# Kernel tuning notes

Hardware: AMD Instinct MI355X
Metric: run time of the kernel (lower is better)

## Reference

```python
import jax, jax.numpy as jnp
import numpy as np
import math

V, B, C, H, W, D, G, N = 4, 2, 32, 128, 128, 32, 8, 4
ATTN_TEMP = 2.0


def _bilinear_sample(img, gx, gy):
    """img: (C,Hs,Ws); gx,gy: (P,) normalized coords in [-1,1].
    PyTorch grid_sample(mode=bilinear, padding=zeros, align_corners=True)."""
    Cc, Hs, Ws = img.shape
    x = (gx + 1.0) * 0.5 * (Ws - 1)
    y = (gy + 1.0) * 0.5 * (Hs - 1)
    x0 = jnp.floor(x)
    y0 = jnp.floor(y)
    wx = x - x0
    wy = y - y0
    x0i = x0.astype(jnp.int32)
    y0i = y0.astype(jnp.int32)

    def gather(xi, yi):
        valid = ((xi >= 0) & (xi < Ws) & (yi >= 0) & (yi < Hs)).astype(img.dtype)
        v = img[:, jnp.clip(yi, 0, Hs - 1), jnp.clip(xi, 0, Ws - 1)]
        return v * valid

    v00 = gather(x0i, y0i)
    v01 = gather(x0i + 1, y0i)
    v10 = gather(x0i, y0i + 1)
    v11 = gather(x0i + 1, y0i + 1)
    return (v00 * (1 - wx) + v01 * wx) * (1 - wy) + (v10 * (1 - wx) + v11 * wx) * wy


_bilinear_batched = jax.vmap(_bilinear_sample)  # over batch


def _homo_warp(src_fea, src_proj, ref_proj, depth):
    """src_fea (B,C,Hs,Ws), projs (B,4,4), depth (B,D,H,W) -> (B,C,D,H,W)."""
    Bb, Cc, Hs, Ws = src_fea.shape
    Dd, Hr, Wr = depth.shape[1], depth.shape[2], depth.shape[3]
    proj = src_proj @ jnp.linalg.inv(ref_proj)
    rot = proj[:, :3, :3]
    trans = proj[:, :3, 3]  # (B,3)
    yy, xx = jnp.meshgrid(jnp.arange(Hr, dtype=jnp.float32),
                          jnp.arange(Wr, dtype=jnp.float32), indexing='ij')
    xyz = jnp.stack([xx.ravel(), yy.ravel(), jnp.ones(Hr * Wr, jnp.float32)], 0)  # (3,P)
    rot_xyz = jnp.einsum('bij,jp->bip', rot, xyz)  # (B,3,P)
    pts = rot_xyz[:, :, None, :] * depth.reshape(Bb, 1, Dd, Hr * Wr) \
          + trans[:, :, None, None]  # (B,3,D,P)
    z = pts[:, 2]
    z = jnp.where(z == 0.0, 1e-9, z)
    gx = pts[:, 0] / z / ((Ws - 1) / 2.0) - 1.0  # (B,D,P)
    gy = pts[:, 1] / z / ((Hs - 1) / 2.0) - 1.0
    # grid built under torch.no_grad in the original
    gx = jax.lax.stop_gradient(gx).reshape(Bb, Dd * Hr * Wr)
    gy = jax.lax.stop_gradient(gy).reshape(Bb, Dd * Hr * Wr)
    warped = _bilinear_batched(src_fea, gx, gy)  # (B,C,D*P)
    return warped.reshape(Bb, Cc, Dd, Hr, Wr)


def setup_inputs() -> dict:
    key = jax.random.key(0)
    ks = jax.random.split(key, 6)
    ref_features = jax.random.normal(ks[0], (V, B, C, H, W), jnp.float32)
    src_features = jax.random.normal(ks[1], (V, B, C, H, W), jnp.float32)
    # structured camera matrices: [.,.,0]=extrinsic, [.,.,1]=intrinsic
    f = 100.0
    K = np.eye(4, dtype=np.float32)
    K[0, 0] = f; K[1, 1] = f; K[0, 2] = W / 2.0; K[1, 2] = H / 2.0
    projs = np.zeros((B, V + 1, 2, 4, 4), np.float32)
    for v in range(V + 1):
        ang = 0.0 if v == 0 else 0.02 * v
        ca, sa = math.cos(ang), math.sin(ang)
        E = np.eye(4, dtype=np.float32)
        E[:3, :3] = np.array([[ca, 0, sa], [0, 1, 0], [-sa, 0, ca]], np.float32)
        E[0, 3] = 0.0 if v == 0 else 5.0 * v
        projs[:, v, 0] = E
        projs[:, v, 1] = K
    proj_matrices = jnp.asarray(projs)
    dvals = jnp.linspace(425.0, 935.0, D, dtype=jnp.float32)
    depth_hypo = dvals[None, :, None, None] * jnp.ones((B, D, H, W), jnp.float32)
    sample_grids = 2.0 * jax.random.uniform(ks[2], (V, B, N, H, W, 2), jnp.float32) - 1.0
    w_reg = jax.random.normal(ks[3], (G,), jnp.float32) * 0.1
    w_enh = jax.random.normal(ks[4], (G, G * N), jnp.float32) * 0.05
    return {
        'ref_features': ref_features,
        'src_features': src_features,
        'proj_matrices': proj_matrices,
        'depth_hypo': depth_hypo,
        'sample_grids': sample_grids,
        'w_reg': w_reg,
        'w_enh': w_enh,
        'group_cor_dim': G,
        'stage_idx': 3,
    }


def reference(ref_features, src_features, proj_matrices, depth_hypo,
              sample_grids, w_reg, w_enh, group_cor_dim, stage_idx):
    Bb, Dd, Hh, Ww = depth_hypo.shape
    Cc = ref_features.shape[2]
    Gg = group_cor_dim
    ref_proj = proj_matrices[:, 0]
    ref_proj_new = ref_proj[:, 0].at[:, :3, :4].set(
        jnp.einsum('bij,bjk->bik', ref_proj[:, 1, :3, :3], ref_proj[:, 0, :3, :4]))
    cor_weight_sum = 1e-8
    cor_feats = 0.0
    cor_weights = []
    for src_idx in range(V):
        src_proj = proj_matrices[:, src_idx + 1]
        src_proj_new = src_proj[:, 0].at[:, :3, :4].set(
            jnp.einsum('bij,bjk->bik', src_proj[:, 1, :3, :3], src_proj[:, 0, :3, :4]))
        warped_src = _homo_warp(src_features[src_idx], src_proj_new, ref_proj_new,
                                depth_hypo)  # (B,C,D,H,W)
        ref_vol = ref_features[src_idx][:, :, None].reshape(Bb, Gg, Cc // Gg, 1, Hh, Ww)
        wsrc = warped_src.reshape(Bb, Gg, Cc // Gg, Dd, Hh, Ww)
        cor_feat = (wsrc * ref_vol).mean(2)  # (B,G,D,H,W) group correlation
        # --- regcorr: second grid_sample along epipolar-line samples ---
        cf = cor_feat.reshape(Bb, Gg * Dd, Hh, Ww)
        grids = sample_grids[src_idx].reshape(Bb, N * Hh * Ww, 2)
        cf_s = _bilinear_batched(cf, grids[..., 0], grids[..., 1])  # (B,G*D,N*H*W)
        cf_s = cf_s.reshape(Bb, Gg, Dd, N, Hh, Ww)
        cf_s = jnp.transpose(cf_s, (0, 1, 3, 2, 4, 5)).reshape(Bb, Gg * N, Dd, Hh, Ww)
        # line_cross_enhanced_net stand-in: learned mix of line samples, residual add
        cor_feat = cor_feat + jnp.einsum('gk,bkdhw->bgdhw', w_enh, cf_s)
        # --- attn_fuse_d softmax fusion across depth ---
        cor_weight = jax.nn.softmax(cor_feat.sum(1) / ATTN_TEMP, axis=1) / math.sqrt(Cc)
        cor_weight_sum = cor_weight_sum + cor_weight
        cor_weights.append(cor_weight.max(1))
        cor_feats = cor_feats + cor_weight[:, None] * cor_feat
    cor_feats = cor_feats / cor_weight_sum[:, None]
    # regnet stand-in: linear reduction over group dim
    attn_logits = jnp.einsum('g,bgdhw->bdhw', w_reg, cor_feats)
    attn_weight = jax.nn.softmax(attn_logits, axis=1)
    idx = jnp.argmax(attn_weight, axis=1)  # (B,H,W)
    depth = jnp.take_along_axis(depth_hypo, idx[:, None], axis=1)[:, 0]
    # stage_idx=3 -> interpolate scale_factor=1 (identity)
    photometric_confidence = attn_weight.max(1)
    return depth, photometric_confidence, attn_weight, jnp.stack(cor_weights)
```

## Files before the change

kernel.cpp:

```cpp
#include <hip/hip_runtime.h>

#define Vv 4
#define Bn 2
#define Cn 32
#define Hn 128
#define Wn 128
#define Dn 32
#define Gn 8
#define Nn 4
#define HW (Hn*Wn)
#define BHW (Bn*Hn*Wn)
#define DHW (Dn*Hn*Wn)
#define BDHW (Bn*Dn*Hn*Wn)
#define NBLK (DHW/256)
#define RBLK (Gn*HW/256)

__global__ void setup_proj(const float* __restrict__ pm,
                           const float* __restrict__ wenh,
                           const float* __restrict__ wreg,
                           double* __restrict__ projws,
                           double* __restrict__ wtab) {
    int t = threadIdx.x;
    if (t < Gn) wtab[t] = (double)wreg[t];
    if (t < Gn * Nn) {
        double a = 0.0, c = 0.0;
        for (int g = 0; g < Gn; g++) {
            double wv = (double)wenh[g * (Gn * Nn) + t];
            a += wv;
            c += (double)wreg[g] * wv;
        }
        wtab[8 + t] = a; wtab[40 + t] = c;
    }
    if (t >= Vv * Bn) return;
    int v = t / Bn, b = t % Bn;
    const float* Eref = pm + (((size_t)b * (Vv + 1) + 0) * 2 + 0) * 16;
    const float* Kref = pm + (((size_t)b * (Vv + 1) + 0) * 2 + 1) * 16;
    const float* Esrc = pm + (((size_t)b * (Vv + 1) + (v + 1)) * 2 + 0) * 16;
    const float* Ksrc = pm + (((size_t)b * (Vv + 1) + (v + 1)) * 2 + 1) * 16;
    double R[16], S[16];
    for (int r = 0; r < 3; r++)
        for (int c = 0; c < 4; c++) {
            R[r*4+c] = (double)Kref[r*4+0]*Eref[0*4+c] + (double)Kref[r*4+1]*Eref[1*4+c] + (double)Kref[r*4+2]*Eref[2*4+c];
            S[r*4+c] = (double)Ksrc[r*4+0]*Esrc[0*4+c] + (double)Ksrc[r*4+1]*Esrc[1*4+c] + (double)Ksrc[r*4+2]*Esrc[2*4+c];
        }
    for (int c = 0; c < 4; c++) { R[12+c] = Eref[12+c]; S[12+c] = Esrc[12+c]; }
    double M[4][8];
    for (int r = 0; r < 4; r++)
        for (int c = 0; c < 4; c++) { M[r][c] = R[r*4+c]; M[r][4+c] = (r == c) ? 1.0 : 0.0; }
    for (int col = 0; col < 4; col++) {
        int piv = col; double best = fabs(M[col][col]);
        for (int r = col+1; r < 4; r++) { double a = fabs(M[r][col]); if (a > best) { best = a; piv = r; } }
        if (piv != col)
            for (int c = 0; c < 8; c++) { double tmp = M[col][c]; M[col][c] = M[piv][c]; M[piv][c] = tmp; }
        double inv = 1.0 / M[col][col];
        for (int c = 0; c < 8; c++) M[col][c] *= inv;
        for (int r = 0; r < 4; r++) if (r != col) {
            double f = M[r][col];
            for (int c = 0; c < 8; c++) M[r][c] -= f * M[col][c];
        }
    }
    double P[16];
    for (int r = 0; r < 4; r++)
        for (int c = 0; c < 4; c++) {
            double acc = 0.0;
            for (int k = 0; k < 4; k++) acc += S[r*4+k] * M[k][4+c];
            P[r*4+c] = acc;
        }
    double* o = projws + t * 12;
    o[0]=P[0];  o[1]=P[1];  o[2]=P[2];
    o[3]=P[4];  o[4]=P[5];  o[5]=P[6];
    o[6]=P[8];  o[7]=P[9];  o[8]=P[10];
    o[9]=P[3];  o[10]=P[7]; o[11]=P[11];
}

__device__ __forceinline__ void repack_body(
    int tid, const float* __restrict__ srcf, const float* __restrict__ reff,
    float4* __restrict__ qsrc, float4* __restrict__ qref, int v, int b)
{
    int p = tid & (HW - 1);
    int g = tid >> 14;
    const float* sb = srcf + ((size_t)(v*Bn + b)) * Cn * HW + (size_t)(g*4) * HW + p;
    const float* rb = reff + ((size_t)(v*Bn + b)) * Cn * HW + (size_t)(g*4) * HW + p;
    float4 s4; s4.x = sb[0]; s4.y = sb[HW]; s4.z = sb[2*HW]; s4.w = sb[3*HW];
    float4 r4; r4.x = rb[0]; r4.y = rb[HW]; r4.z = rb[2*HW]; r4.w = rb[3*HW];
    qsrc[(size_t)g * HW + p] = s4;
    qref[(size_t)g * HW + p] = r4;
}

__device__ __forceinline__ void warp_body_q(
    int tid, const float4* __restrict__ qsrc, const float4* __restrict__ qref,
    const float* __restrict__ dh, const double* __restrict__ projws,
    const float* sU1, const float* sU2, const float* sR,
    float2* __restrict__ ownbuf, float2* __restrict__ tapbuf, int v, int b)
{
    int d = tid & 31, p = tid >> 5;
    int w = p & 127, h = p >> 7;
    const double* pr = projws + (v * Bn + b) * 12;
    double depth = (double)dh[(size_t)(b * Dn + d) * HW + p];
    double xf = (double)w, yf = (double)h;
    double px = (pr[0]*xf + pr[1]*yf + pr[2]) * depth + pr[9];
    double py = (pr[3]*xf + pr[4]*yf + pr[5]) * depth + pr[10];
    double pz = (pr[6]*xf + pr[7]*yf + pr[8]) * depth + pr[11];
    if (pz == 0.0) pz = 1e-9;
    double invz = 1.0 / pz;
    double xs = px * invz;
    double ys = py * invz;
    double x0f = floor(xs), y0f = floor(ys);
    double wx = xs - x0f, wy = ys - y0f;
    int ix = (int)x0f, iy = (int)y0f;
    bool vx0 = (ix >= 0) && (ix < Wn), vx1 = (ix + 1 >= 0) && (ix + 1 < Wn);
    bool vy0 = (iy >= 0) && (iy < Hn), vy1 = (iy + 1 >= 0) && (iy + 1 < Hn);
    int cx0 = min(max(ix, 0), Wn-1), cx1 = min(max(ix+1, 0), Wn-1);
    int cy0 = min(max(iy, 0), Hn-1), cy1 = min(max(iy+1, 0), Hn-1);
    float a00 = (vx0 && vy0) ? (float)((1.0-wx)*(1.0-wy)) : 0.f;
    float a01 = (vx1 && vy0) ? (float)(wx*(1.0-wy))       : 0.f;
    float a10 = (vx0 && vy1) ? (float)((1.0-wx)*wy)       : 0.f;
    float a11 = (vx1 && vy1) ? (float)(wx*wy)             : 0.f;
    int o00 = cy0*Wn + cx0, o01 = cy0*Wn + cx1, o10 = cy1*Wn + cx0, o11 = cy1*Wn + cx1;
    float cor[Gn];
    #pragma unroll
    for (int j = 0; j < Gn; j++) {
        const float4* qs = qsrc + (size_t)j * HW;
        float4 t00 = qs[o00], t01 = qs[o01], t10 = qs[o10], t11 = qs[o11];
        float4 rr = qref[(size_t)j * HW + p];
        float vx = a00*t00.x + a01*t01.x + a10*t10.x + a11*t11.x;
        float vy = a00*t00.y + a01*t01.y + a10*t10.y + a11*t11.y;
        float vz = a00*t00.z + a01*t01.z + a10*t10.z + a11*t11.z;
        float vw = a00*t00.w + a01*t01.w + a10*t10.w + a11*t11.w;
        cor[j] = ((vx*rr.x + vy*rr.y) + vz*rr.z) + vw*rr.w;
    }
    float s_own = 0.f, r_own = 0.f;
    #pragma unroll
    for (int g = 0; g < Gn; g++) { s_own += cor[g]; r_own += sR[g] * cor[g]; }
    float2 o2; o2.x = 0.25f * s_own; o2.y = 0.25f * r_own;
    ownbuf[tid] = o2;
    #pragma unroll
    for (int n = 0; n < Nn; n++) {
        float t1 = 0.f, t2 = 0.f;
        #pragma unroll
        for (int g = 0; g < Gn; g++) {
            t1 += sU1[g*Nn + n] * cor[g];
            t2 += sU2[g*Nn + n] * cor[g];
        }
        float2 t; t.x = 0.25f * t1; t.y = 0.25f * t2;
        tapbuf[((size_t)p * Nn + n) * Dn + d] = t;
    }
}

__device__ __forceinline__ void warp_body(
    int tid, const float* __restrict__ srcf, const float* __restrict__ reff,
    const float* __restrict__ dh, const double* __restrict__ projws,
    const float* sU1, const float* sU2, const float* sR,
    float2* __restrict__ ownbuf, float2* __restrict__ tapbuf, int v, int b)
{
    int d = tid & 31, p = tid >> 5;
    int w = p & 127, h = p >> 7;
    const double* pr = projws + (v * Bn + b) * 12;
    double depth = (double)dh[(size_t)(b * Dn + d) * HW + p];
    double xf = (double)w, yf = (double)h;
    double px = (pr[0]*xf + pr[1]*yf + pr[2]) * depth + pr[9];
    double py = (pr[3]*xf + pr[4]*yf + pr[5]) * depth + pr[10];
    double pz = (pr[6]*xf + pr[7]*yf + pr[8]) * depth + pr[11];
    if (pz == 0.0) pz = 1e-9;
    double invz = 1.0 / pz;
    double xs = px * invz;
    double ys = py * invz;
    double x0f = floor(xs), y0f = floor(ys);
    double wx = xs - x0f, wy = ys - y0f;
    int ix = (int)x0f, iy = (int)y0f;
    bool vx0 = (ix >= 0) && (ix < Wn), vx1 = (ix + 1 >= 0) && (ix + 1 < Wn);
    bool vy0 = (iy >= 0) && (iy < Hn), vy1 = (iy + 1 >= 0) && (iy + 1 < Hn);
    int cx0 = min(max(ix, 0), Wn-1), cx1 = min(max(ix+1, 0), Wn-1);
    int cy0 = min(max(iy, 0), Hn-1), cy1 = min(max(iy+1, 0), Hn-1);
    float a00 = (vx0 && vy0) ? (float)((1.0-wx)*(1.0-wy)) : 0.f;
    float a01 = (vx1 && vy0) ? (float)(wx*(1.0-wy))       : 0.f;
    float a10 = (vx0 && vy1) ? (float)((1.0-wx)*wy)       : 0.f;
    float a11 = (vx1 && vy1) ? (float)(wx*wy)             : 0.f;
    int o00 = cy0*Wn + cx0, o01 = cy0*Wn + cx1, o10 = cy1*Wn + cx0, o11 = cy1*Wn + cx1;
    const float* sb = srcf + ((size_t)(v*Bn + b)) * Cn * HW;
    const float* rb = reff + ((size_t)(v*Bn + b)) * Cn * HW + p;
    float cor[Gn];
    #pragma unroll
    for (int g = 0; g < Gn; g++) cor[g] = 0.f;
    #pragma unroll
    for (int c = 0; c < Cn; c++) {
        const float* sc = sb + c * HW;
        float val = a00*sc[o00] + a01*sc[o01] + a10*sc[o10] + a11*sc[o11];
        cor[c >> 2] += val * rb[c * HW];
    }
    float s_own = 0.f, r_own = 0.f;
    #pragma unroll
    for (int g = 0; g < Gn; g++) { s_own += cor[g]; r_own += sR[g] * cor[g]; }
    float2 o2; o2.x = 0.25f * s_own; o2.y = 0.25f * r_own;
    ownbuf[tid] = o2;
    #pragma unroll
    for (int n = 0; n < Nn; n++) {
        float t1 = 0.f, t2 = 0.f;
        #pragma unroll
        for (int g = 0; g < Gn; g++) {
            t1 += sU1[g*Nn + n] * cor[g];
            t2 += sU2[g*Nn + n] * cor[g];
        }
        float2 t; t.x = 0.25f * t1; t.y = 0.25f * t2;
        tapbuf[((size_t)p * Nn + n) * Dn + d] = t;
    }
}

template <int MODE>
__device__ __forceinline__ void sample_body(
    int tid, const float2* __restrict__ ownbuf, const float2* __restrict__ tapbuf,
    const float* __restrict__ grids, float2* __restrict__ accf,
    float* __restrict__ out_corw, const float* __restrict__ depth_hypo,
    float* __restrict__ out, int v, int b)
{
    int d = tid & 31;
    int p = tid >> 5;
    int w = p & 127, h = p >> 7;

    float2 ow = ownbuf[tid];
    double s = (double)ow.x, r = (double)ow.y;

    const float2* gb2 = (const float2*)(grids + ((size_t)(v*Bn + b)) * Nn * HW * 2);
    #pragma unroll
    for (int n = 0; n < Nn; n++) {
        float2 g2 = gb2[((size_t)n * Hn + h) * Wn + w];
        double gx = (double)g2.x, gy = (double)g2.y;
        double xs = (gx + 1.0) * 63.5;
        double ys = (gy + 1.0) * 63.5;
        double x0f = floor(xs), y0f = floor(ys);
        double wx = xs - x0f, wy = ys - y0f;
        int ix = (int)x0f, iy = (int)y0f;
        bool vx0 = (ix >= 0) && (ix < Wn), vx1 = (ix + 1 >= 0) && (ix + 1 < Wn);
        bool vy0 = (iy >= 0) && (iy < Hn), vy1 = (iy + 1 >= 0) && (iy + 1 < Hn);
        int cx0 = min(max(ix, 0), Wn-1), cx1 = min(max(ix+1, 0), Wn-1);
        int cy0 = min(max(iy, 0), Hn-1), cy1 = min(max(iy+1, 0), Hn-1);
        double a00 = (vx0 && vy0) ? (1.0-wx)*(1.0-wy) : 0.0;
        double a01 = (vx1 && vy0) ? wx*(1.0-wy)       : 0.0;
        double a10 = (vx0 && vy1) ? (1.0-wx)*wy       : 0.0;
        double a11 = (vx1 && vy1) ? wx*wy             : 0.0;
        float2 q00 = tapbuf[((size_t)(cy0*Wn + cx0) * Nn + n) * Dn + d];
        float2 q01 = tapbuf[((size_t)(cy0*Wn + cx1) * Nn + n) * Dn + d];
        float2 q10 = tapbuf[((size_t)(cy1*Wn + cx0) * Nn + n) * Dn + d];
        float2 q11 = tapbuf[((size_t)(cy1*Wn + cx1) * Nn + n) * Dn + d];
        s += a00*(double)q00.x + a01*(double)q01.x + a10*(double)q10.x + a11*(double)q11.x;
        r += a00*(double)q00.y + a01*(double)q01.y + a10*(double)q10.y + a11*(double)q11.y;
    }
    double logit = s * 0.5;
    double m = logit;
    #pragma unroll
    for (int mask = 16; mask >= 1; mask >>= 1) m = fmax(m, __shfl_xor(m, mask));
    double e = exp(logit - m);
    double ssum = e;
    #pragma unroll
    for (int mask = 16; mask >= 1; mask >>= 1) ssum += __shfl_xor(ssum, mask);
    const double SQRTC = 5.656854249492381;
    double cw = e / ssum / SQRTC;
    if (d == 0) out_corw[(size_t)v * BHW + (size_t)b * HW + p] = (float)(1.0 / ssum / SQRTC);

    if (MODE == 0) {
        float2 a; a.x = (float)(1e-8 + cw); a.y = (float)(cw * r);
        accf[tid] = a;
    } else if (MODE == 1) {
        float2 a = accf[tid];
        a.x = (float)((double)a.x + cw);
        a.y = (float)((double)a.y + cw * r);
        accf[tid] = a;
    } else {
        float2 a = accf[tid];
        double cs = (double)a.x + cw;
        double wr = (double)a.y + cw * r;
        double lg = wr / cs;
        double fm = lg;
        #pragma unroll
        for (int mask = 16; mask >= 1; mask >>= 1) fm = fmax(fm, __shfl_xor(fm, mask));
        double fe = exp(lg - fm);
        double fsum = fe;
        #pragma unroll
        for (int mask = 16; mask >= 1; mask >>= 1) fsum += __shfl_xor(fsum, mask);
        out[2*BHW + (size_t)b * DHW + (size_t)d * HW + p] = (float)(fe / fsum);
        double bv = lg; int bi = d;
        #pragma unroll
        for (int mask = 16; mask >= 1; mask >>= 1) {
            double ov = __shfl_xor(bv, mask);
            int oi = __shfl_xor(bi, mask);
            if (ov > bv || (ov == bv && oi < bi)) { bv = ov; bi = oi; }
        }
        double rv = (d == bi) ? -1e300 : lg; int ri = d;
        #pragma unroll
        for (int mask = 16; mask >= 1; mask >>= 1) {
            double ov = __shfl_xor(rv, mask);
            int oi = __shfl_xor(ri, mask);
            if (ov > rv || (ov == rv && oi < ri)) { rv = ov; ri = oi; }
        }
        if (d == 0) {
            const float* dhb = depth_hypo + (size_t)b * DHW + p;
            double eps = 5e-3 * (1.0 + fabs(bv));
            bool adj = (ri == bi + 1) || (ri == bi - 1);
            float dep;
            if (adj && (bv - rv) <= eps)
                dep = 0.5f * (dhb[(size_t)bi * HW] + dhb[(size_t)ri * HW]);
            else
                dep = dhb[(size_t)bi * HW];
            out[(size_t)b * HW + p] = dep;
            out[BHW + (size_t)b * HW + p] = (float)(1.0 / fsum);
        }
    }
}

__global__ __launch_bounds__(256) void repack_k(
    const float* __restrict__ srcf, const float* __restrict__ reff,
    float4* __restrict__ qsrc, float4* __restrict__ qref, int v, int b)
{
    repack_body(blockIdx.x * 256 + threadIdx.x, srcf, reff, qsrc, qref, v, b);
}

__global__ __launch_bounds__(256) void warp0_q(
    const float* __restrict__ srcf, const float* __restrict__ reff,
    const float4* __restrict__ qsrcR, const float4* __restrict__ qrefR,
    float4* __restrict__ qsrcW, float4* __restrict__ qrefW,
    const float* __restrict__ dh, const double* __restrict__ projws,
    const double* __restrict__ wtab,
    float2* __restrict__ ownbuf, float2* __restrict__ tapbuf)
{
    int lt = threadIdx.x;
    if (blockIdx.x < NBLK) {
        __shared__ float sU1[Gn * Nn], sU2[Gn * Nn], sR[Gn];
        if (lt < Gn * Nn) { sU1[lt] = (float)wtab[8 + lt]; sU2[lt] = (float)wtab[40 + lt]; }
        if (lt < Gn) sR[lt] = (float)wtab[lt];
        __syncthreads();
        warp_body_q(blockIdx.x * 256 + lt, qsrcR, qrefR, dh, projws,
                    sU1, sU2, sR, ownbuf, tapbuf, 0, 0);
    } else {
        repack_body((blockIdx.x - NBLK) * 256 + lt, srcf, reff, qsrcW, qrefW, 1, 0);
    }
}

__global__ __launch_bounds__(256) void warp_corr(
    const float* __restrict__ srcf, const float* __restrict__ reff,
    const float* __restrict__ dh, const double* __restrict__ projws,
    const double* __restrict__ wtab,
    float2* __restrict__ ownbuf, float2* __restrict__ tapbuf, int v, int b)
{
    __shared__ float sU1[Gn * Nn], sU2[Gn * Nn], sR[Gn];
    int lt = threadIdx.x;
    if (lt < Gn * Nn) { sU1[lt] = (float)wtab[8 + lt]; sU2[lt] = (float)wtab[40 + lt]; }
    if (lt < Gn) sR[lt] = (float)wtab[lt];
    __syncthreads();
    warp_body(blockIdx.x * 256 + lt, srcf, reff, dh, projws, sU1, sU2, sR,
              ownbuf, tapbuf, v, b);
}

template <int MODE>
__global__ __launch_bounds__(256) void sample_enh(
    const float2* __restrict__ ownbuf, const float2* __restrict__ tapbuf,
    const float* __restrict__ grids, float2* __restrict__ accf,
    float* __restrict__ out_corw, const float* __restrict__ depth_hypo,
    float* __restrict__ out, int v, int b)
{
    sample_body<MODE>(blockIdx.x * 256 + threadIdx.x, ownbuf, tapbuf, grids,
                      accf, out_corw, depth_hypo, out, v, b);
}

template <int MODE>
__global__ __launch_bounds__(256) void fused_swq(
    const float* __restrict__ srcf, const float* __restrict__ reff,
    const float4* __restrict__ qsrcR, const float4* __restrict__ qrefR,
    float4* __restrict__ qsrcW, float4* __restrict__ qrefW,
    const float* __restrict__ dh, const double* __restrict__ projws,
    const double* __restrict__ wtab, const float* __restrict__ grids,
    const float2* __restrict__ ownR, const float2* __restrict__ tapR,
    float2* __restrict__ ownW, float2* __restrict__ tapW,
    float2* __restrict__ accf, float* __restrict__ out_corw,
    float* __restrict__ out, int vs, int bs, int vw, int bw, int vr, int br)
{
    int lt = threadIdx.x;
    if (blockIdx.x >= 2*NBLK) {
        repack_body((blockIdx.x - 2*NBLK) * 256 + lt, srcf, reff, qsrcW, qrefW, vr, br);
        return;
    }
    int role = blockIdx.x & 1;
    int vb   = blockIdx.x >> 1;
    if (role == 0) {
        sample_body<MODE>(vb * 256 + lt, ownR, tapR, grids,
                          accf, out_corw, dh, out, vs, bs);
    } else {
        __shared__ float sU1[Gn * Nn], sU2[Gn * Nn], sR[Gn];
        if (lt < Gn * Nn) { sU1[lt] = (float)wtab[8 + lt]; sU2[lt] = (float)wtab[40 + lt]; }
        if (lt < Gn) sR[lt] = (float)wtab[lt];
        __syncthreads();
        warp_body_q(vb * 256 + lt, qsrcR, qrefR, dh, projws,
                    sU1, sU2, sR, ownW, tapW, vw, bw);
    }
}

template <int MODE>
__global__ __launch_bounds__(256) void fused_sw(
    const float* __restrict__ srcf, const float* __restrict__ reff,
    const float* __restrict__ dh, const double* __restrict__ projws,
    const double* __restrict__ wtab, const float* __restrict__ grids,
    const float2* __restrict__ ownR, const float2* __restrict__ tapR,
    float2* __restrict__ ownW, float2* __restrict__ tapW,
    float2* __restrict__ accf, float* __restrict__ out_corw,
    float* __restrict__ out, int vs, int bs, int vw, int bw)
{
    int lt = threadIdx.x;
    int role = blockIdx.x & 1;
    int vb   = blockIdx.x >> 1;
    if (role == 0) {
        sample_body<MODE>(vb * 256 + lt, ownR, tapR, grids,
                          accf, out_corw, dh, out, vs, bs);
    } else {
        __shared__ float sU1[Gn * Nn], sU2[Gn * Nn], sR[Gn];
        if (lt < Gn * Nn) { sU1[lt] = (float)wtab[8 + lt]; sU2[lt] = (float)wtab[40 + lt]; }
        if (lt < Gn) sR[lt] = (float)wtab[lt];
        __syncthreads();
        warp_body(vb * 256 + lt, srcf, reff, dh, projws,
                  sU1, sU2, sR, ownW, tapW, vw, bw);
    }
}

extern "C" void kernel_launch(void* const* d_in, const int* in_sizes, int n_in,
                              void* d_out, int out_size, void* d_ws, size_t ws_size,
                              hipStream_t stream) {
    const float* reff  = (const float*)d_in[0];
    const float* srcf  = (const float*)d_in[1];
    const float* pm    = (const float*)d_in[2];
    const float* dh    = (const float*)d_in[3];
    const float* grids = (const float*)d_in[4];
    const float* wreg  = (const float*)d_in[5];
    const float* wenh  = (const float*)d_in[6];
    float* out = (float*)d_out;
    double* projws = (double*)d_ws;
    double* wtab   = (double*)((char*)d_ws + 1024);
    float2* accf   = (float2*)((char*)d_ws + 2048);
    float2* own0   = accf + DHW;
    float2* tap0   = own0 + DHW;
    float2* own1   = tap0 + (size_t)DHW * Nn;
    float2* tap1   = own1 + DHW;
    float4* q0s    = (float4*)(tap1 + (size_t)DHW * Nn);
    float4* q0r    = q0s + (size_t)Gn * HW;
    float4* q1s    = q0r + (size_t)Gn * HW;
    float4* q1r    = q1s + (size_t)Gn * HW;
    size_t need_pipe  = 2048 + (size_t)DHW * 8 + 2 * ((size_t)DHW * 8 + (size_t)DHW * Nn * 8);
    size_t need_pipe2 = need_pipe + 4 * (size_t)Gn * HW * 16;
    bool pipe2 = (ws_size >= need_pipe2);
    bool pipe  = (ws_size >= need_pipe);

    setup_proj<<<1, 64, 0, stream>>>(pm, wenh, wreg, projws, wtab);
    float* out_corw = out + 2*BHW + BDHW;

    if (pipe2) {
        float2* owns[2] = { own0, own1 };
        float2* taps[2] = { tap0, tap1 };
        float4* qs[2]   = { q0s, q1s };
        float4* qr[2]   = { q0r, q1r };
        repack_k<<<RBLK, 256, 0, stream>>>(srcf, reff, q0s, q0r, 0, 0);
        warp0_q<<<NBLK + RBLK, 256, 0, stream>>>(srcf, reff, q0s, q0r, q1s, q1r,
                                                 dh, projws, wtab, own0, tap0);
        for (int k = 1; k < 8; k++) {
            int vs = (k - 1) & 3, bs = (k - 1) >> 2;
            int vw = k & 3,       bw = k >> 2;
            int vr = (k + 1) & 3, br = (k + 1) >> 2;
            bool rep = (k <= 6);
            int grid = 2*NBLK + (rep ? RBLK : 0);
            float2* oR = owns[(k - 1) & 1]; float2* tR = taps[(k - 1) & 1];
            float2* oW = owns[k & 1];       float2* tW = taps[k & 1];
            const float4* qsR = qs[k & 1];  const float4* qrR = qr[k & 1];
            float4* qsW = qs[(k + 1) & 1];  float4* qrW = qr[(k + 1) & 1];
            if (vs == 0)
                fused_swq<0><<<grid, 256, 0, stream>>>(srcf, reff, qsR, qrR, qsW, qrW,
                                                       dh, projws, wtab, grids,
                                                       oR, tR, oW, tW, accf, out_corw,
                                                       out, vs, bs, vw, bw, vr, br);
            else if (vs == 3)
                fused_swq<2><<<grid, 256, 0, stream>>>(srcf, reff, qsR, qrR, qsW, qrW,
                                                       dh, projws, wtab, grids,
                                                       oR, tR, oW, tW, accf, out_corw,
                                                       out, vs, bs, vw, bw, vr, br);
            else
                fused_swq<1><<<grid, 256, 0, stream>>>(srcf, reff, qsR, qrR, qsW, qrW,
                                                       dh, projws, wtab, grids,
                                                       oR, tR, oW, tW, accf, out_corw,
                                                       out, vs, bs, vw, bw, vr, br);
        }
        sample_enh<2><<<NBLK, 256, 0, stream>>>(owns[1], taps[1], grids, accf,
                                                out_corw, dh, out, 3, 1);
    } else if (pipe) {
        float2* owns[2] = { own0, own1 };
        float2* taps[2] = { tap0, tap1 };
        warp_corr<<<NBLK, 256, 0, stream>>>(srcf, reff, dh, projws, wtab,
                                            own0, tap0, 0, 0);
        for (int k = 1; k < 8; k++) {
            int vs = (k - 1) & 3, bs = (k - 1) >> 2;
            int vw = k & 3,       bw = k >> 2;
            float2* oR = owns[(k - 1) & 1]; float2* tR = taps[(k - 1) & 1];
            float2* oW = owns[k & 1];       float2* tW = taps[k & 1];
            if (vs == 0)
                fused_sw<0><<<2*NBLK, 256, 0, stream>>>(srcf, reff, dh, projws, wtab, grids,
                                                        oR, tR, oW, tW, accf,
                                                        out_corw, out, vs, bs, vw, bw);
            else if (vs == 3)
                fused_sw<2><<<2*NBLK, 256, 0, stream>>>(srcf, reff, dh, projws, wtab, grids,
                                                        oR, tR, oW, tW, accf,
                                                        out_corw, out, vs, bs, vw, bw);
            else
                fused_sw<1><<<2*NBLK, 256, 0, stream>>>(srcf, reff, dh, projws, wtab, grids,
                                                        oR, tR, oW, tW, accf,
                                                        out_corw, out, vs, bs, vw, bw);
        }
        sample_enh<2><<<NBLK, 256, 0, stream>>>(owns[1], taps[1], grids, accf,
                                                out_corw, dh, out, 3, 1);
    } else {
        for (int b = 0; b < Bn; b++) {
            for (int v = 0; v < Vv; v++) {
                warp_corr<<<NBLK, 256, 0, stream>>>(srcf, reff, dh, projws, wtab,
                                                    own0, tap0, v, b);
                if (v == 0)
                    sample_enh<0><<<NBLK, 256, 0, stream>>>(own0, tap0, grids, accf,
                                                            out_corw, dh, out, v, b);
                else if (v < Vv - 1)
                    sample_enh<1><<<NBLK, 256, 0, stream>>>(own0, tap0, grids, accf,
                                                            out_corw, dh, out, v, b);
                else
                    sample_enh<2><<<NBLK, 256, 0, stream>>>(own0, tap0, grids, accf,
                                                            out_corw, dh, out, v, b);
            }
        }
    }
}
```

Baseline: 229.7 us.

## Batch all view-batch stages into three large kernels instead of pipelined chain

Replaces the 9-launch double-buffered pipeline (repack/warp/sample per view-batch pair) with three kernels that process all 8 view-batch slices at once: a batched repack, a batched warp, and a single sample kernel that loops over the 4 views per pixel and finalizes in registers. This removes per-step launch overhead and the accf read-modify-write between views, and gives each launch a much larger grid. In exchange it needs a far larger workspace holding all own/tap buffers (~8x), which raises memory footprint and traffic; if the workspace is too small it falls back to the older path.

```diff
diff --git a/kernel.cpp b/kernel.cpp
--- a/kernel.cpp
+++ b/kernel.cpp
@@ -14,6 +14,7 @@
 #define BDHW (Bn*Dn*Hn*Wn)
 #define NBLK (DHW/256)
 #define RBLK (Gn*HW/256)
+#define NST  (Vv*Bn)
 
 __global__ void setup_proj(const float* __restrict__ pm,
                            const float* __restrict__ wenh,
@@ -206,20 +207,14 @@
     }
 }
 
-template <int MODE>
-__device__ __forceinline__ void sample_body(
-    int tid, const float2* __restrict__ ownbuf, const float2* __restrict__ tapbuf,
-    const float* __restrict__ grids, float2* __restrict__ accf,
-    float* __restrict__ out_corw, const float* __restrict__ depth_hypo,
-    float* __restrict__ out, int v, int b)
-{
-    int d = tid & 31;
-    int p = tid >> 5;
-    int w = p & 127, h = p >> 7;
-
-    float2 ow = ownbuf[tid];
+__device__ __forceinline__ void sample_view(
+    int d, int p, int w, int h,
+    const float2* __restrict__ ownbuf, const float2* __restrict__ tapbuf,
+    const float* __restrict__ grids, float* __restrict__ out_corw,
+    int v, int b, double& cw_out, double& r_out)
+{
+    float2 ow = ownbuf[(size_t)p * Dn + d];
     double s = (double)ow.x, r = (double)ow.y;
-
     const float2* gb2 = (const float2*)(grids + ((size_t)(v*Bn + b)) * Nn * HW * 2);
     #pragma unroll
     for (int n = 0; n < Nn; n++) {
@@ -254,9 +249,117 @@
     #pragma unroll
     for (int mask = 16; mask >= 1; mask >>= 1) ssum += __shfl_xor(ssum, mask);
     const double SQRTC = 5.656854249492381;
-    double cw = e / ssum / SQRTC;
     if (d == 0) out_corw[(size_t)v * BHW + (size_t)b * HW + p] = (float)(1.0 / ssum / SQRTC);
-
+    cw_out = e / ssum / SQRTC;
+    r_out = r;
+}
+
+__device__ __forceinline__ void finalize_core(
+    int d, int p, int b, double cs, double wr,
+    const float* __restrict__ depth_hypo, float* __restrict__ out)
+{
+    double lg = wr / cs;
+    double fm = lg;
+    #pragma unroll
+    for (int mask = 16; mask >= 1; mask >>= 1) fm = fmax(fm, __shfl_xor(fm, mask));
+    double fe = exp(lg - fm);
+    double fsum = fe;
+    #pragma unroll
+    for (int mask = 16; mask >= 1; mask >>= 1) fsum += __shfl_xor(fsum, mask);
+    out[2*BHW + (size_t)b * DHW + (size_t)d * HW + p] = (float)(fe / fsum);
+    double bv = lg; int bi = d;
+    #pragma unroll
+    for (int mask = 16; mask >= 1; mask >>= 1) {
+        double ov = __shfl_xor(bv, mask);
+        int oi = __shfl_xor(bi, mask);
+        if (ov > bv || (ov == bv && oi < bi)) { bv = ov; bi = oi; }
+    }
+    double rv = (d == bi) ? -1e300 : lg; int ri = d;
+    #pragma unroll
+    for (int mask = 16; mask >= 1; mask >>= 1) {
+        double ov = __shfl_xor(rv, mask);
+        int oi = __shfl_xor(ri, mask);
+        if (ov > rv || (ov == rv && oi < ri)) { rv = ov; ri = oi; }
+    }
+    if (d == 0) {
+        const float* dhb = depth_hypo + (size_t)b * DHW + p;
+        double eps = 5e-3 * (1.0 + fabs(bv));
+        bool adj = (ri == bi + 1) || (ri == bi - 1);
+        float dep;
+        if (adj && (bv - rv) <= eps)
+            dep = 0.5f * (dhb[(size_t)bi * HW] + dhb[(size_t)ri * HW]);
+        else
+            dep = dhb[(size_t)bi * HW];
+        out[(size_t)b * HW + p] = dep;
+        out[BHW + (size_t)b * HW + p] = (float)(1.0 / fsum);
+    }
+}
+
+__global__ __launch_bounds__(256) void mega_repack(
+    const float* __restrict__ srcf, const float* __restrict__ reff,
+    float4* __restrict__ qs_all, float4* __restrict__ qr_all)
+{
+    int s = blockIdx.x >> 9;
+    int tid = (blockIdx.x & 511) * 256 + threadIdx.x;
+    int v = s & 3, b = s >> 2;
+    mega_repack_body: ;
+    repack_body(tid, srcf, reff, qs_all + (size_t)s * Gn * HW,
+                qr_all + (size_t)s * Gn * HW, v, b);
+}
+
+__global__ __launch_bounds__(256) void mega_warp(
+    const float4* __restrict__ qs_all, const float4* __restrict__ qr_all,
+    const float* __restrict__ dh, const double* __restrict__ projws,
+    const double* __restrict__ wtab,
+    float2* __restrict__ own_all, float2* __restrict__ tap_all)
+{
+    __shared__ float sU1[Gn * Nn], sU2[Gn * Nn], sR[Gn];
+    int lt = threadIdx.x;
+    if (lt < Gn * Nn) { sU1[lt] = (float)wtab[8 + lt]; sU2[lt] = (float)wtab[40 + lt]; }
+    if (lt < Gn) sR[lt] = (float)wtab[lt];
+    __syncthreads();
+    int s = blockIdx.x >> 11;
+    int tid = (blockIdx.x & 2047) * 256 + lt;
+    int v = s & 3, b = s >> 2;
+    warp_body_q(tid, qs_all + (size_t)s * Gn * HW, qr_all + (size_t)s * Gn * HW,
+                dh, projws, sU1, sU2, sR,
+                own_all + (size_t)s * DHW, tap_all + (size_t)s * Nn * DHW, v, b);
+}
+
+__global__ __launch_bounds__(256) void mega_sample(
+    const float2* __restrict__ own_all, const float2* __restrict__ tap_all,
+    const float* __restrict__ grids, const float* __restrict__ dh,
+    float* __restrict__ out_corw, float* __restrict__ out)
+{
+    int tid = blockIdx.x * 256 + threadIdx.x;
+    int d = tid & 31;
+    int p = (tid >> 5) & (HW - 1);
+    int b = tid >> 19;
+    int w = p & 127, h = p >> 7;
+    double cs = 1e-8, wr = 0.0;
+    for (int v = 0; v < Vv; v++) {
+        int s = b * 4 + v;
+        double cw, r;
+        sample_view(d, p, w, h, own_all + (size_t)s * DHW,
+                    tap_all + (size_t)s * Nn * DHW, grids, out_corw, v, b, cw, r);
+        cs += cw;
+        wr += cw * r;
+    }
+    finalize_core(d, p, b, cs, wr, dh, out);
+}
+
+template <int MODE>
+__device__ __forceinline__ void sample_body(
+    int tid, const float2* __restrict__ ownbuf, const float2* __restrict__ tapbuf,
+    const float* __restrict__ grids, float2* __restrict__ accf,
+    float* __restrict__ out_corw, const float* __restrict__ depth_hypo,
+    float* __restrict__ out, int v, int b)
+{
+    int d = tid & 31;
+    int p = tid >> 5;
+    int w = p & 127, h = p >> 7;
+    double cw, r;
+    sample_view(d, p, w, h, ownbuf, tapbuf, grids, out_corw, v, b, cw, r);
     if (MODE == 0) {
         float2 a; a.x = (float)(1e-8 + cw); a.y = (float)(cw * r);
         accf[tid] = a;
@@ -267,71 +370,7 @@
         accf[tid] = a;
     } else {
         float2 a = accf[tid];
-        double cs = (double)a.x + cw;
-        double wr = (double)a.y + cw * r;
-        double lg = wr / cs;
-        double fm = lg;
-        #pragma unroll
-        for (int mask = 16; mask >= 1; mask >>= 1) fm = fmax(fm, __shfl_xor(fm, mask));
-        double fe = exp(lg - fm);
-        double fsum = fe;
-        #pragma unroll
-        for (int mask = 16; mask >= 1; mask >>= 1) fsum += __shfl_xor(fsum, mask);
-        out[2*BHW + (size_t)b * DHW + (size_t)d * HW + p] = (float)(fe / fsum);
-        double bv = lg; int bi = d;
-        #pragma unroll
-        for (int mask = 16; mask >= 1; mask >>= 1) {
-            double ov = __shfl_xor(bv, mask);
-            int oi = __shfl_xor(bi, mask);
-            if (ov > bv || (ov == bv && oi < bi)) { bv = ov; bi = oi; }
-        }
-        double rv = (d == bi) ? -1e300 : lg; int ri = d;
-        #pragma unroll
-        for (int mask = 16; mask >= 1; mask >>= 1) {
-            double ov = __shfl_xor(rv, mask);
-            int oi = __shfl_xor(ri, mask);
-            if (ov > rv || (ov == rv && oi < ri)) { rv = ov; ri = oi; }
-        }
-        if (d == 0) {
-            const float* dhb = depth_hypo + (size_t)b * DHW + p;
-            double eps = 5e-3 * (1.0 + fabs(bv));
-            bool adj = (ri == bi + 1) || (ri == bi - 1);
-            float dep;
-            if (adj && (bv - rv) <= eps)
-                dep = 0.5f * (dhb[(size_t)bi * HW] + dhb[(size_t)ri * HW]);
-            else
-                dep = dhb[(size_t)bi * HW];
-            out[(size_t)b * HW + p] = dep;
-            out[BHW + (size_t)b * HW + p] = (float)(1.0 / fsum);
-        }
-    }
-}
-
-__global__ __launch_bounds__(256) void repack_k(
-    const float* __restrict__ srcf, const float* __restrict__ reff,
-    float4* __restrict__ qsrc, float4* __restrict__ qref, int v, int b)
-{
-    repack_body(blockIdx.x * 256 + threadIdx.x, srcf, reff, qsrc, qref, v, b);
-}
-
-__global__ __launch_bounds__(256) void warp0_q(
-    const float* __restrict__ srcf, const float* __restrict__ reff,
-    const float4* __restrict__ qsrcR, const float4* __restrict__ qrefR,
-    float4* __restrict__ qsrcW, float4* __restrict__ qrefW,
-    const float* __restrict__ dh, const double* __restrict__ projws,
-    const double* __restrict__ wtab,
-    float2* __restrict__ ownbuf, float2* __restrict__ tapbuf)
-{
-    int lt = threadIdx.x;
-    if (blockIdx.x < NBLK) {
-        __shared__ float sU1[Gn * Nn], sU2[Gn * Nn], sR[Gn];
-        if (lt < Gn * Nn) { sU1[lt] = (float)wtab[8 + lt]; sU2[lt] = (float)wtab[40 + lt]; }
-        if (lt < Gn) sR[lt] = (float)wtab[lt];
-        __syncthreads();
-        warp_body_q(blockIdx.x * 256 + lt, qsrcR, qrefR, dh, projws,
-                    sU1, sU2, sR, ownbuf, tapbuf, 0, 0);
-    } else {
-        repack_body((blockIdx.x - NBLK) * 256 + lt, srcf, reff, qsrcW, qrefW, 1, 0);
+        finalize_core(d, p, b, (double)a.x + cw, (double)a.y + cw * r, depth_hypo, out);
     }
 }
 
@@ -359,38 +398,6 @@
 {
     sample_body<MODE>(blockIdx.x * 256 + threadIdx.x, ownbuf, tapbuf, grids,
                       accf, out_corw, depth_hypo, out, v, b);
-}
-
-template <int MODE>
-__global__ __launch_bounds__(256) void fused_swq(
-    const float* __restrict__ srcf, const float* __restrict__ reff,
-    const float4* __restrict__ qsrcR, const float4* __restrict__ qrefR,
-    float4* __restrict__ qsrcW, float4* __restrict__ qrefW,
-    const float* __restrict__ dh, const double* __restrict__ projws,
-    const double* __restrict__ wtab, const float* __restrict__ grids,
-    const float2* __restrict__ ownR, const float2* __restrict__ tapR,
-    float2* __restrict__ ownW, float2* __restrict__ tapW,
-    float2* __restrict__ accf, float* __restrict__ out_corw,
-    float* __restrict__ out, int vs, int bs, int vw, int bw, int vr, int br)
-{
-    int lt = threadIdx.x;
-    if (blockIdx.x >= 2*NBLK) {
-        repack_body((blockIdx.x - 2*NBLK) * 256 + lt, srcf, reff, qsrcW, qrefW, vr, br);
-        return;
-    }
-    int role = blockIdx.x & 1;
-    int vb   = blockIdx.x >> 1;
-    if (role == 0) {
-        sample_body<MODE>(vb * 256 + lt, ownR, tapR, grids,
-                          accf, out_corw, dh, out, vs, bs);
-    } else {
-        __shared__ float sU1[Gn * Nn], sU2[Gn * Nn], sR[Gn];
-        if (lt < Gn * Nn) { sU1[lt] = (float)wtab[8 + lt]; sU2[lt] = (float)wtab[40 + lt]; }
-        if (lt < Gn) sR[lt] = (float)wtab[lt];
-        __syncthreads();
-        warp_body_q(vb * 256 + lt, qsrcR, qrefR, dh, projws,
-                    sU1, sU2, sR, ownW, tapW, vw, bw);
-    }
 }
 
 template <int MODE>
@@ -432,60 +439,30 @@
     float* out = (float*)d_out;
     double* projws = (double*)d_ws;
     double* wtab   = (double*)((char*)d_ws + 1024);
-    float2* accf   = (float2*)((char*)d_ws + 2048);
-    float2* own0   = accf + DHW;
-    float2* tap0   = own0 + DHW;
-    float2* own1   = tap0 + (size_t)DHW * Nn;
-    float2* tap1   = own1 + DHW;
-    float4* q0s    = (float4*)(tap1 + (size_t)DHW * Nn);
-    float4* q0r    = q0s + (size_t)Gn * HW;
-    float4* q1s    = q0r + (size_t)Gn * HW;
-    float4* q1r    = q1s + (size_t)Gn * HW;
-    size_t need_pipe  = 2048 + (size_t)DHW * 8 + 2 * ((size_t)DHW * 8 + (size_t)DHW * Nn * 8);
-    size_t need_pipe2 = need_pipe + 4 * (size_t)Gn * HW * 16;
-    bool pipe2 = (ws_size >= need_pipe2);
-    bool pipe  = (ws_size >= need_pipe);
+    char*   base   = (char*)d_ws + 2048;
+    float2* tap_all = (float2*)base;
+    float2* own_all = tap_all + (size_t)NST * Nn * DHW;
+    float4* qs_all  = (float4*)(own_all + (size_t)NST * DHW);
+    float4* qr_all  = qs_all + (size_t)NST * Gn * HW;
+    size_t need_mega = 2048 + (size_t)NST * Nn * DHW * 8 + (size_t)NST * DHW * 8
+                     + 2 * (size_t)NST * Gn * HW * 16;
+    float2* accf = (float2*)base;
+    float2* own0 = accf + DHW;
+    float2* tap0 = own0 + DHW;
+    float2* own1 = tap0 + (size_t)DHW * Nn;
+    float2* tap1 = own1 + DHW;
+    size_t need_pipe = 2048 + (size_t)DHW * 8 + 2 * ((size_t)DHW * 8 + (size_t)DHW * Nn * 8);
 
     setup_proj<<<1, 64, 0, stream>>>(pm, wenh, wreg, projws, wtab);
     float* out_corw = out + 2*BHW + BDHW;
 
-    if (pipe2) {
-        float2* owns[2] = { own0, own1 };
-        float2* taps[2] = { tap0, tap1 };
-        float4* qs[2]   = { q0s, q1s };
-        float4* qr[2]   = { q0r, q1r };
-        repack_k<<<RBLK, 256, 0, stream>>>(srcf, reff, q0s, q0r, 0, 0);
-        warp0_q<<<NBLK + RBLK, 256, 0, stream>>>(srcf, reff, q0s, q0r, q1s, q1r,
-                                                 dh, projws, wtab, own0, tap0);
-        for (int k = 1; k < 8; k++) {
-            int vs = (k - 1) & 3, bs = (k - 1) >> 2;
-            int vw = k & 3,       bw = k >> 2;
-            int vr = (k + 1) & 3, br = (k + 1) >> 2;
-            bool rep = (k <= 6);
-            int grid = 2*NBLK + (rep ? RBLK : 0);
-            float2* oR = owns[(k - 1) & 1]; float2* tR = taps[(k - 1) & 1];
-            float2* oW = owns[k & 1];       float2* tW = taps[k & 1];
-            const float4* qsR = qs[k & 1];  const float4* qrR = qr[k & 1];
-            float4* qsW = qs[(k + 1) & 1];  float4* qrW = qr[(k + 1) & 1];
-            if (vs == 0)
-                fused_swq<0><<<grid, 256, 0, stream>>>(srcf, reff, qsR, qrR, qsW, qrW,
-                                                       dh, projws, wtab, grids,
-                                                       oR, tR, oW, tW, accf, out_corw,
-                                                       out, vs, bs, vw, bw, vr, br);
-            else if (vs == 3)
-                fused_swq<2><<<grid, 256, 0, stream>>>(srcf, reff, qsR, qrR, qsW, qrW,
-                                                       dh, projws, wtab, grids,
-                                                       oR, tR, oW, tW, accf, out_corw,
-                                                       out, vs, bs, vw, bw, vr, br);
-            else
-                fused_swq<1><<<grid, 256, 0, stream>>>(srcf, reff, qsR, qrR, qsW, qrW,
-                                                       dh, projws, wtab, grids,
-                                                       oR, tR, oW, tW, accf, out_corw,
-                                                       out, vs, bs, vw, bw, vr, br);
-        }
-        sample_enh<2><<<NBLK, 256, 0, stream>>>(owns[1], taps[1], grids, accf,
-                                                out_corw, dh, out, 3, 1);
-    } else if (pipe) {
+    if (ws_size >= need_mega) {
+        mega_repack<<<NST * RBLK, 256, 0, stream>>>(srcf, reff, qs_all, qr_all);
+        mega_warp<<<NST * NBLK, 256, 0, stream>>>(qs_all, qr_all, dh, projws, wtab,
+                                                  own_all, tap_all);
+        mega_sample<<<BDHW / 256, 256, 0, stream>>>(own_all, tap_all, grids, dh,
+                                                    out_corw, out);
+    } else if (ws_size >= need_pipe) {
         float2* owns[2] = { own0, own1 };
         float2* taps[2] = { tap0, tap1 };
         warp_corr<<<NBLK, 256, 0, stream>>>(srcf, reff, dh, projws, wtab,
```

After: 192.7 us. 1.19x faster.
